# Kernel tuning notes

Hardware: AMD Instinct MI355X
Metric: run time of the kernel (lower is better)

The kernel has to match this reference:

```python
import jax, jax.numpy as jnp
import numpy as np

NUM_RBF = 16
TOP_K = 32
MAX_REL = 32  # max_relative_feature


def _rbf(D):
    # D: [...,] -> [..., NUM_RBF]
    mu = jnp.linspace(2.0, 22.0, NUM_RBF)
    sigma = (22.0 - 2.0) / NUM_RBF
    return jnp.exp(-(((D[..., None] - mu) / sigma) ** 2))


def _gather_nodes(x, idx):
    # x: [B, N, ...], idx: [B, N, K] -> [B, N, K, ...]
    return jax.vmap(lambda xb, ib: xb[ib])(x, idx)


def _forward(X, mask, residue_idx, chain_labels, W_pos, b_pos, W_edge, ln_gamma, ln_beta):
    N_at = X[:, :, 0, :]
    C = X[:, :, 1, :]
    Ca = X[:, :, 2, :]
    O = X[:, :, 3, :]
    b = Ca - N_at
    c = C - Ca
    a = jnp.cross(b, c)
    Cb = -0.58273431 * a + 0.56802827 * b - 0.54067466 * c + Ca

    # --- _dist: masked pairwise distances on C atoms + topk neighbor search ---
    mask2 = mask[:, :, None] * mask[:, None, :]              # [B,N,N]
    dX = C[:, None, :, :] - C[:, :, None, :]                 # [B,N,N,3]
    D = mask2 * jnp.sqrt(jnp.sum(dX ** 2, -1) + 1e-6)
    D_max = jnp.max(D, -1, keepdims=True)
    D_adjust = D + (1.0 - mask2) * D_max
    neg_vals, E_idx = jax.lax.top_k(-D_adjust, TOP_K)        # smallest distances
    D_neighbors = -neg_vals                                  # [B,N,K]

    # --- 25 RBF distance features (1 from topk + 24 atom-pair gathers) ---
    atoms = {'N': N_at, 'C': C, 'Ca': Ca, 'Cb': Cb, 'O': O}
    pairs = [('N','N'),('Ca','Ca'),('Cb','Cb'),('C','N'),('C','Ca'),('C','Cb'),
             ('N','Ca'),('N','Cb'),('Cb','Ca'),('N','C'),('Ca','C'),('Cb','C'),
             ('Ca','N'),('Cb','N'),('Ca','Cb'),('O','O'),('C','O'),('O','C'),
             ('N','O'),('O','N'),('Cb','O'),('O','Ca'),('O','Cb'),('Ca','O')]
    A_all = jnp.stack([atoms[p[0]] for p in pairs])          # [P,B,N,3]
    B_all = jnp.stack([atoms[p[1]] for p in pairs])          # [P,B,N,3]
    B_nb = jax.vmap(_gather_nodes, in_axes=(0, None))(B_all, E_idx)  # [P,B,N,K,3]
    D_pair = jnp.sqrt(jnp.sum((A_all[:, :, :, None, :] - B_nb) ** 2, -1) + 1e-6)  # [P,B,N,K]
    RBF_pairs = _rbf(D_pair)                                 # [P,B,N,K,R]
    Bsz, Nres, K = E_idx.shape
    RBF_all = jnp.concatenate(
        [_rbf(D_neighbors), jnp.moveaxis(RBF_pairs, 0, 3).reshape(Bsz, Nres, K, -1)], -1)

    # --- positional encodings (relative residue index, chain mask) ---
    r_nb = _gather_nodes(residue_idx, E_idx)                 # [B,N,K]
    offset = residue_idx[:, :, None] - r_nb
    c_nb = _gather_nodes(chain_labels, E_idx)
    E_chains = (chain_labels[:, :, None] == c_nb).astype(jnp.int32)
    d = jnp.clip(offset + MAX_REL, 0, 2 * MAX_REL) * E_chains + (1 - E_chains) * (2 * MAX_REL + 1)
    E_pos = W_pos[d] + b_pos                                 # one_hot @ W == table lookup

    # --- edge embedding + LayerNorm ---
    E = jnp.concatenate([E_pos, RBF_all], -1)                # [B,N,K,416]
    E = E @ W_edge                                           # [B,N,K,128]
    mu = jnp.mean(E, -1, keepdims=True)
    var = jnp.var(E, -1, keepdims=True)
    E = (E - mu) / jnp.sqrt(var + 1e-5) * ln_gamma + ln_beta
    return E, E_idx


def setup_inputs() -> dict:
    key = jax.random.key(0)
    ks = jax.random.split(key, 6)
    B, N = 4, 2048
    edge_in = 16 + NUM_RBF * 25  # 416
    X = jax.random.normal(ks[0], (B, N, 4, 3), dtype=jnp.float32) * 10.0
    mask = jnp.ones((B, N), dtype=jnp.float32)
    residue_idx = jnp.broadcast_to(jnp.arange(N, dtype=jnp.int32), (B, N))
    chain_labels = jax.random.randint(ks[1], (B, N), 0, 2).astype(jnp.int32)
    W_pos = jax.random.normal(ks[2], (2 * MAX_REL + 2, 16), dtype=jnp.float32) * 0.05
    b_pos = jnp.zeros((16,), dtype=jnp.float32)
    W_edge = jax.random.normal(ks[3], (edge_in, 128), dtype=jnp.float32) * 0.05
    ln_gamma = jnp.ones((128,), dtype=jnp.float32)
    ln_beta = jnp.zeros((128,), dtype=jnp.float32)
    return {"X": X, "mask": mask, "residue_idx": residue_idx, "chain_labels": chain_labels,
            "W_pos": W_pos, "b_pos": b_pos, "W_edge": W_edge,
            "ln_gamma": ln_gamma, "ln_beta": ln_beta}


def reference(X, mask, residue_idx, chain_labels, W_pos, b_pos, W_edge, ln_gamma, ln_beta):
    return _forward(X, mask, residue_idx, chain_labels, W_pos, b_pos, W_edge, ln_gamma, ln_beta)
```

## Files before the change

### kernel.cpp

```cpp
#include <hip/hip_runtime.h>
#include <math.h>

#define BB 4
#define NN 2048
#define KK 32
#define COUT 128
#define KT 13
#define NBIN 512
#define SCAP 512
#define TGN 4096
#define CHA 7
#define CHB 6

typedef __attribute__((ext_vector_type(8))) short bf16x8;
typedef __attribute__((ext_vector_type(4))) float f32x4;
typedef unsigned long long ull;

constexpr int PA_E[12] = {0,3,1,0,3,2,2,2,1,0,3,4};
constexpr int PB_E[12] = {0,3,2,2,2,1,0,3,4,4,4,3};
constexpr int PA_O[12] = {2,1,1,0,0,3,3,4,4,4,4,2};
constexpr int PB_O[12] = {2,0,3,3,1,1,0,4,1,0,2,4};

__device__ inline ushort f2bf(float x) {
    unsigned u = __float_as_uint(x);
    unsigned r = (u + 0x7FFFu + ((u >> 16) & 1u)) >> 16;
    return (ushort)r;
}

__global__ __launch_bounds__(256) void prep_kernel(
    const float* __restrict__ X, const float* __restrict__ W,
    const float* __restrict__ Wpos, const float* __restrict__ bpos,
    ushort* __restrict__ Wsw, uint4* __restrict__ rbfTab,
    ushort* __restrict__ WposBf, float4* __restrict__ Ccomp) {
    int blk = blockIdx.x, tid = threadIdx.x;
    if (blk < 26) {
        int t = blk * 256 + tid;
        int lane = t & 63;
        int ct = (t >> 6) & 7;
        int kt = t >> 9;
        int k0 = kt * 32 + (lane >> 4) * 8;
        int col = ct * 16 + (lane & 15);
        ushort o[8];
#pragma unroll
        for (int i = 0; i < 8; i++) o[i] = f2bf(W[(k0 + i) * COUT + col]);
        *reinterpret_cast<uint4*>(Wsw + (size_t)t * 8) = *reinterpret_cast<uint4*>(o);
    } else if (blk < 42) {
        int g = (blk - 26) * 256 + tid;
        float d = ((float)g + 0.5f) * (1.0f / 128.0f);
        unsigned w[8];
#pragma unroll
        for (int i2 = 0; i2 < 8; i2++) {
            float mu0 = 2.0f + (20.0f / 15.0f) * (float)(2 * i2);
            float mu1 = 2.0f + (20.0f / 15.0f) * (float)(2 * i2 + 1);
            float u0 = (d - mu0) * 0.8f;
            float u1 = (d - mu1) * 0.8f;
            float e0 = __expf(-u0 * u0);
            float e1 = __expf(-u1 * u1);
            w[i2] = ((__float_as_uint(e0) + 0x8000u) >> 16) |
                    ((__float_as_uint(e1) + 0x8000u) & 0xFFFF0000u);
        }
        rbfTab[g * 2 + 0] = make_uint4(w[0], w[1], w[2], w[3]);
        rbfTab[g * 2 + 1] = make_uint4(w[4], w[5], w[6], w[7]);
    } else if (blk < 47) {
        int t = (blk - 42) * 256 + tid;
        if (t < 66 * 16) {
            int c = t & 15;
            WposBf[t] = f2bf(Wpos[t] + bpos[c]);
        }
    } else {
        int i = (blk - 47) * 256 + tid;
        const float4* p4 = (const float4*)(X + (size_t)i * 12);
        float4 f0 = p4[0], f1 = p4[1];
        Ccomp[i] = make_float4(f0.w, f1.x, f1.y, 0.0f);
    }
}

__global__ __launch_bounds__(256) void topk_kernel(const float4* __restrict__ Ccomp,
                                                   int* __restrict__ eidx,
                                                   float* __restrict__ dnb,
                                                   float* __restrict__ out_idx) {
    __shared__ unsigned hist[NBIN];
    __shared__ ull surv[SCAP];
    __shared__ unsigned wcnt[4][8];
    int bid = blockIdx.x;
    int b = bid >> 11;
    int n = bid & (NN - 1);
    int tid = threadIdx.x;
    const int wv = tid >> 6, lane = tid & 63;

    hist[tid] = 0;
    hist[tid + 256] = 0;
    __syncthreads();

    const float4* cb = Ccomp + (size_t)b * NN;
    float4 s = cb[n];
    ull key[8];
    int bin[8];
#pragma unroll
    for (int i = 0; i < 8; i++) {
        int j = i * 256 + tid;
        float4 c = cb[j];
        float dx = c.x - s.x, dy = c.y - s.y, dz = c.z - s.z;
        float d = sqrtf(dx * dx + dy * dy + dz * dz + 1e-6f);
        key[i] = ((ull)__float_as_uint(d) << 32) | (unsigned)j;
        bin[i] = (int)fminf(d * 8.0f, (float)(NBIN - 1));
        atomicAdd(&hist[bin[i]], 1u);
    }
    __syncthreads();

    if (tid < 64) {
        int base = tid * 8;
        unsigned h[8];
        unsigned tot = 0;
#pragma unroll
        for (int i = 0; i < 8; i++) { h[i] = hist[base + i]; tot += h[i]; }
        unsigned sc = tot;
#pragma unroll
        for (int off = 1; off <= 32; off <<= 1) {
            unsigned o = __shfl_up(sc, off);
            if (tid >= off) sc += o;
        }
        unsigned run = sc - tot;
#pragma unroll
        for (int i = 0; i < 8; i++) {
            unsigned c = h[i];
            hist[base + i] = run;
            run += c;
        }
    }
    __syncthreads();

    ull blt[8];
#pragma unroll
    for (int i = 0; i < 8; i++) {
        blt[i] = __ballot(hist[bin[i]] < KK);
    }
    if (lane == 0) {
#pragma unroll
        for (int i = 0; i < 8; i++) wcnt[wv][i] = (unsigned)__popcll(blt[i]);
    }
    __syncthreads();

    unsigned mybase[8];
    unsigned run = 0;
#pragma unroll
    for (int i = 0; i < 8; i++) {
#pragma unroll
        for (int w = 0; w < 4; w++) {
            if (w == wv) mybase[i] = run;
            run += wcnt[w][i];
        }
    }
    const ull ltm = (1ULL << lane) - 1ULL;
#pragma unroll
    for (int i = 0; i < 8; i++) {
        if (hist[bin[i]] < KK) {
            unsigned pos = mybase[i] + (unsigned)__popcll(blt[i] & ltm);
            if (pos < SCAP) surv[pos] = key[i];
        }
    }
    int sv = (int)(run < SCAP ? run : SCAP);
    __syncthreads();

    for (int i = tid; i < sv; i += 256) {
        ull k = surv[i];
        int rank = 0;
        for (int t = 0; t < sv; ++t) rank += (surv[t] < k) ? 1 : 0;
        if (rank < KK) {
            int j = (int)(unsigned)(k & 0xffffffffu);
            float d = __uint_as_float((unsigned)(k >> 32));
            size_t o = (size_t)bid * KK + rank;
            eidx[o] = j;
            dnb[o] = d;
            out_idx[o] = (float)j;
        }
    }
}

__global__ __launch_bounds__(512, 4) void edge_kernel(
    const float* __restrict__ X, const int* __restrict__ eidx,
    const float* __restrict__ dnb, const int* __restrict__ ridx,
    const int* __restrict__ clab, const ushort* __restrict__ WposBf,
    const ushort* __restrict__ Wsw, const uint4* __restrict__ rbfTab,
    const float* __restrict__ gamma, const float* __restrict__ beta,
    float* __restrict__ Eout, float* __restrict__ outIdx) {
    __shared__ ushort wbuf[CHA * 4096];

    const int tid = threadIdx.x;
    const int wv = tid >> 6, lane = tid & 63;
    const int node = blockIdx.x * 8 + wv;
    const int bbase = node & ~(NN - 1);
    const int q = lane >> 4, r = lane & 15;
    const int h = q & 1, par = q >> 1;

    auto stage = [&](int k0, int nk) {
        for (int p = 0; p < nk; p++) {
            const ushort* src = Wsw + (k0 + p) * 4096 + tid * 8;
            ushort* dst = &wbuf[p * 4096 + wv * 512];
            __builtin_amdgcn_global_load_lds(
                (const __attribute__((address_space(1))) unsigned int*)src,
                (__attribute__((address_space(3))) unsigned int*)dst, 16, 0, 0);
        }
    };
    stage(0, CHA);

    const int erow0 = node * KK + r;
    const int erow1 = node * KK + 16 + r;
    const int j0 = eidx[(size_t)erow0];
    const int j1 = eidx[(size_t)erow1];

    auto loadAtoms = [&](int i, float* A) {
        const float4* p4 = (const float4*)(X + (size_t)i * 12);
        float4 f0 = p4[0], f1 = p4[1], f2 = p4[2];
        A[0] = f0.x;  A[1] = f0.y;  A[2] = f0.z;
        A[3] = f0.w;  A[4] = f1.x;  A[5] = f1.y;
        A[6] = f1.z;  A[7] = f1.w;  A[8] = f2.x;
        A[12] = f2.y; A[13] = f2.z; A[14] = f2.w;
        float bx = A[6] - A[0], by = A[7] - A[1], bz = A[8] - A[2];
        float cx = A[3] - A[6], cy = A[4] - A[7], cz = A[5] - A[8];
        float ax = by * cz - bz * cy;
        float ay = bz * cx - bx * cz;
        float az = bx * cy - by * cx;
        A[9]  = -0.58273431f * ax + 0.56802827f * bx - 0.54067466f * cx + A[6];
        A[10] = -0.58273431f * ay + 0.56802827f * by - 0.54067466f * cy + A[7];
        A[11] = -0.58273431f * az + 0.56802827f * bz - 0.54067466f * cz + A[8];
        A[15] = 0.0f;
    };
    float S[16], R0[16], R1[16];
    loadAtoms(node, S);
    loadAtoms(bbase + j0, R0);
    loadAtoms(bbase + j1, R1);

    float d0[12], d1[12];
#define DIST12(PAx, PBx)                                                          \
    {                                                                             \
        _Pragma("unroll") for (int t = 0; t < 12; t++) {                          \
            const int ia = PAx[t] * 3, ib = PBx[t] * 3;                           \
            float dx = S[ia] - R0[ib], dy = S[ia + 1] - R0[ib + 1],               \
                  dz = S[ia + 2] - R0[ib + 2];                                    \
            d0[t] = sqrtf(dx * dx + dy * dy + dz * dz + 1e-6f);                   \
            dx = S[ia] - R1[ib]; dy = S[ia + 1] - R1[ib + 1];                     \
            dz = S[ia + 2] - R1[ib + 2];                                          \
            d1[t] = sqrtf(dx * dx + dy * dy + dz * dz + 1e-6f);                   \
        }                                                                         \
    }
    if (par == 0) DIST12(PA_E, PB_E) else DIST12(PA_O, PB_O)
#undef DIST12

    union U8 { uint4 u4; bf16x8 v; };
    auto rbf8 = [&](float d) -> bf16x8 {
        int idx = (int)fminf(d * 128.0f, (float)(TGN - 1));
        U8 o;
        o.u4 = rbfTab[idx * 2 + h];
        return o.v;
    };
    bf16x8 a00, a10;
    if (q < 2) {
        int off0 = ridx[node] - ridx[bbase + j0];
        int dd0 = off0 + 32; dd0 = dd0 < 0 ? 0 : (dd0 > 64 ? 64 : dd0);
        int dpos0 = (clab[node] == clab[bbase + j0]) ? dd0 : 65;
        int off1 = ridx[node] - ridx[bbase + j1];
        int dd1 = off1 + 32; dd1 = dd1 < 0 ? 0 : (dd1 > 64 ? 64 : dd1);
        int dpos1 = (clab[node] == clab[bbase + j1]) ? dd1 : 65;
        U8 aE0, aE1;
        aE0.u4 = *(const uint4*)(WposBf + dpos0 * 16 + 8 * h);
        aE1.u4 = *(const uint4*)(WposBf + dpos1 * 16 + 8 * h);
        a00 = aE0.v; a10 = aE1.v;
    } else {
        a00 = rbf8(dnb[(size_t)erow0]);
        a10 = rbf8(dnb[(size_t)erow1]);
    }

    f32x4 acc0[8], acc1[8];
#pragma unroll
    for (int ct = 0; ct < 8; ct++) {
        acc0[ct] = (f32x4){0.f, 0.f, 0.f, 0.f};
        acc1[ct] = (f32x4){0.f, 0.f, 0.f, 0.f};
    }
    const ushort* bs = wbuf + lane * 8;
    __syncthreads();
#pragma unroll
    for (int kt = 0; kt < CHA; kt++) {
        bf16x8 a0, a1;
        if (kt == 0) { a0 = a00; a1 = a10; }
        else         { a0 = rbf8(d0[kt - 1]); a1 = rbf8(d1[kt - 1]); }
#pragma unroll
        for (int ct = 0; ct < 8; ct++) {
            bf16x8 w = *(const bf16x8*)(bs + kt * 4096 + ct * 512);
            acc0[ct] = __builtin_amdgcn_mfma_f32_16x16x32_bf16(w, a0, acc0[ct], 0, 0, 0);
            acc1[ct] = __builtin_amdgcn_mfma_f32_16x16x32_bf16(w, a1, acc1[ct], 0, 0, 0);
        }
    }
    __syncthreads();
    stage(CHA, CHB);
    __syncthreads();
#pragma unroll
    for (int kt = CHA; kt < KT; kt++) {
        bf16x8 a0 = rbf8(d0[kt - 1]);
        bf16x8 a1 = rbf8(d1[kt - 1]);
#pragma unroll
        for (int ct = 0; ct < 8; ct++) {
            bf16x8 w = *(const bf16x8*)(bs + (kt - CHA) * 4096 + ct * 512);
            acc0[ct] = __builtin_amdgcn_mfma_f32_16x16x32_bf16(w, a0, acc0[ct], 0, 0, 0);
            acc1[ct] = __builtin_amdgcn_mfma_f32_16x16x32_bf16(w, a1, acc1[ct], 0, 0, 0);
        }
    }

    float s1a = 0.f, s2a = 0.f, s1b = 0.f, s2b = 0.f;
#pragma unroll
    for (int ct = 0; ct < 8; ct++) {
#pragma unroll
        for (int i = 0; i < 4; i++) {
            float v0 = acc0[ct][i];
            float v1 = acc1[ct][i];
            s1a += v0; s2a += v0 * v0;
            s1b += v1; s2b += v1 * v1;
        }
    }
    s1a += __shfl_xor(s1a, 16); s2a += __shfl_xor(s2a, 16);
    s1a += __shfl_xor(s1a, 32); s2a += __shfl_xor(s2a, 32);
    s1b += __shfl_xor(s1b, 16); s2b += __shfl_xor(s2b, 16);
    s1b += __shfl_xor(s1b, 32); s2b += __shfl_xor(s2b, 32);
    float meanA = s1a * (1.0f / 128.0f);
    float varA = s2a * (1.0f / 128.0f) - meanA * meanA;
    float rstdA = rsqrtf(varA + 1e-5f);
    float meanB = s1b * (1.0f / 128.0f);
    float varB = s2b * (1.0f / 128.0f) - meanB * meanB;
    float rstdB = rsqrtf(varB + 1e-5f);

    float* orow0 = Eout + (size_t)erow0 * COUT + q * 4;
    float* orow1 = Eout + (size_t)erow1 * COUT + q * 4;
#pragma unroll
    for (int ct = 0; ct < 8; ct++) {
        float4 g4 = *(const float4*)(gamma + ct * 16 + q * 4);
        float4 b4 = *(const float4*)(beta + ct * 16 + q * 4);
        float4 oa, ob;
        oa.x = (acc0[ct][0] - meanA) * rstdA * g4.x + b4.x;
        oa.y = (acc0[ct][1] - meanA) * rstdA * g4.y + b4.y;
        oa.z = (acc0[ct][2] - meanA) * rstdA * g4.z + b4.z;
        oa.w = (acc0[ct][3] - meanA) * rstdA * g4.w + b4.w;
        ob.x = (acc1[ct][0] - meanB) * rstdB * g4.x + b4.x;
        ob.y = (acc1[ct][1] - meanB) * rstdB * g4.y + b4.y;
        ob.z = (acc1[ct][2] - meanB) * rstdB * g4.z + b4.z;
        ob.w = (acc1[ct][3] - meanB) * rstdB * g4.w + b4.w;
        *(float4*)(orow0 + ct * 16) = oa;
        *(float4*)(orow1 + ct * 16) = ob;
    }

    if (q == 0) {
        outIdx[(size_t)erow0] = (float)j0;
        outIdx[(size_t)erow1] = (float)j1;
    }
}

extern "C" void kernel_launch(void* const* d_in, const int* in_sizes, int n_in,
                              void* d_out, int out_size, void* d_ws, size_t ws_size,
                              hipStream_t stream) {
    const float* X = (const float*)d_in[0];
    const int* ridx = (const int*)d_in[2];
    const int* clab = (const int*)d_in[3];
    const float* Wpos = (const float*)d_in[4];
    const float* bpos = (const float*)d_in[5];
    const float* Wedge = (const float*)d_in[6];
    const float* gamma = (const float*)d_in[7];
    const float* beta = (const float*)d_in[8];

    float* out = (float*)d_out;
    float* E = out;
    float* outidx = out + (size_t)BB * NN * KK * COUT;

    char* ws = (char*)d_ws;
    uint4* rbfTab = (uint4*)ws;
    ushort* Wsw = (ushort*)(ws + 131072);
    ushort* WposBf = (ushort*)(ws + 131072 + 106496);
    float4* Ccomp = (float4*)(ws + 131072 + 106496 + 2112);
    int* eidx = (int*)(ws + 131072 + 106496 + 2112 + 131072);
    float* dnbuf = (float*)(ws + 131072 + 106496 + 2112 + 131072 + 1048576);

    prep_kernel<<<79, 256, 0, stream>>>(X, Wedge, Wpos, bpos, Wsw, rbfTab,
                                        WposBf, Ccomp);
    topk_kernel<<<BB * NN, 256, 0, stream>>>(Ccomp, eidx, dnbuf, outidx);
    edge_kernel<<<BB * NN / 8, 512, 0, stream>>>(X, eidx, dnbuf, ridx, clab,
                                                 WposBf, Wsw, rbfTab, gamma, beta,
                                                 E, outidx);
}
```

Baseline: 90.84 us.

## Overlap weight prep with topk and double-buffer edge kernel weight staging

The weight swizzle, RBF table and positional-table prep move out of the first kernel and into extra blocks at the end of the topk grid, leaving a tiny Ccomp-only kernel on the critical path. In the edge kernel, the second weight chunk goes into a separate LDS buffer and is staged before the first chunk's MFMAs, so its load overlaps compute instead of following a barrier. All RBF table lookups are also hoisted into registers ahead of the MFMA loop. The cost is more LDS and registers per block, with launch bounds lowered from 4 to 2 blocks per CU, which cuts occupancy.

Measured after the change: 103.7 us. +14.2%, slower.

```diff
diff --git a/kernel.cpp b/kernel.cpp
--- a/kernel.cpp
+++ b/kernel.cpp
@@ -9,8 +9,7 @@
 #define NBIN 512
 #define SCAP 512
 #define TGN 4096
-#define CHA 7
-#define CHB 6
+#define NTOPK (BB * NN)
 
 typedef __attribute__((ext_vector_type(8))) short bf16x8;
 typedef __attribute__((ext_vector_type(4))) float f32x4;
@@ -27,65 +26,68 @@
     return (ushort)r;
 }
 
-__global__ __launch_bounds__(256) void prep_kernel(
-    const float* __restrict__ X, const float* __restrict__ W,
+__global__ __launch_bounds__(256) void ccomp_kernel(const float* __restrict__ X,
+                                                    float4* __restrict__ Ccomp) {
+    int i = blockIdx.x * 256 + threadIdx.x;
+    const float4* p4 = (const float4*)(X + (size_t)i * 12);
+    float4 f0 = p4[0], f1 = p4[1];
+    Ccomp[i] = make_float4(f0.w, f1.x, f1.y, 0.0f);
+}
+
+__global__ __launch_bounds__(256) void topk_kernel(
+    const float4* __restrict__ Ccomp, const float* __restrict__ W,
     const float* __restrict__ Wpos, const float* __restrict__ bpos,
     ushort* __restrict__ Wsw, uint4* __restrict__ rbfTab,
-    ushort* __restrict__ WposBf, float4* __restrict__ Ccomp) {
-    int blk = blockIdx.x, tid = threadIdx.x;
-    if (blk < 26) {
-        int t = blk * 256 + tid;
-        int lane = t & 63;
-        int ct = (t >> 6) & 7;
-        int kt = t >> 9;
-        int k0 = kt * 32 + (lane >> 4) * 8;
-        int col = ct * 16 + (lane & 15);
-        ushort o[8];
-#pragma unroll
-        for (int i = 0; i < 8; i++) o[i] = f2bf(W[(k0 + i) * COUT + col]);
-        *reinterpret_cast<uint4*>(Wsw + (size_t)t * 8) = *reinterpret_cast<uint4*>(o);
-    } else if (blk < 42) {
-        int g = (blk - 26) * 256 + tid;
-        float d = ((float)g + 0.5f) * (1.0f / 128.0f);
-        unsigned w[8];
-#pragma unroll
-        for (int i2 = 0; i2 < 8; i2++) {
-            float mu0 = 2.0f + (20.0f / 15.0f) * (float)(2 * i2);
-            float mu1 = 2.0f + (20.0f / 15.0f) * (float)(2 * i2 + 1);
-            float u0 = (d - mu0) * 0.8f;
-            float u1 = (d - mu1) * 0.8f;
-            float e0 = __expf(-u0 * u0);
-            float e1 = __expf(-u1 * u1);
-            w[i2] = ((__float_as_uint(e0) + 0x8000u) >> 16) |
-                    ((__float_as_uint(e1) + 0x8000u) & 0xFFFF0000u);
-        }
-        rbfTab[g * 2 + 0] = make_uint4(w[0], w[1], w[2], w[3]);
-        rbfTab[g * 2 + 1] = make_uint4(w[4], w[5], w[6], w[7]);
-    } else if (blk < 47) {
-        int t = (blk - 42) * 256 + tid;
-        if (t < 66 * 16) {
-            int c = t & 15;
-            WposBf[t] = f2bf(Wpos[t] + bpos[c]);
-        }
-    } else {
-        int i = (blk - 47) * 256 + tid;
-        const float4* p4 = (const float4*)(X + (size_t)i * 12);
-        float4 f0 = p4[0], f1 = p4[1];
-        Ccomp[i] = make_float4(f0.w, f1.x, f1.y, 0.0f);
-    }
-}
-
-__global__ __launch_bounds__(256) void topk_kernel(const float4* __restrict__ Ccomp,
-                                                   int* __restrict__ eidx,
-                                                   float* __restrict__ dnb,
-                                                   float* __restrict__ out_idx) {
+    ushort* __restrict__ WposBf, int* __restrict__ eidx,
+    float* __restrict__ dnb, float* __restrict__ out_idx) {
+    int bid = blockIdx.x;
+    int tid = threadIdx.x;
+
+    if (bid >= NTOPK) {
+        int blk = bid - NTOPK;
+        if (blk < 26) {
+            int t = blk * 256 + tid;
+            int lane = t & 63;
+            int ct = (t >> 6) & 7;
+            int kt = t >> 9;
+            int k0 = kt * 32 + (lane >> 4) * 8;
+            int col = ct * 16 + (lane & 15);
+            ushort o[8];
+#pragma unroll
+            for (int i = 0; i < 8; i++) o[i] = f2bf(W[(k0 + i) * COUT + col]);
+            *reinterpret_cast<uint4*>(Wsw + (size_t)t * 8) = *reinterpret_cast<uint4*>(o);
+        } else if (blk < 42) {
+            int g = (blk - 26) * 256 + tid;
+            float d = ((float)g + 0.5f) * (1.0f / 128.0f);
+            unsigned w[8];
+#pragma unroll
+            for (int i2 = 0; i2 < 8; i2++) {
+                float mu0 = 2.0f + (20.0f / 15.0f) * (float)(2 * i2);
+                float mu1 = 2.0f + (20.0f / 15.0f) * (float)(2 * i2 + 1);
+                float u0 = (d - mu0) * 0.8f;
+                float u1 = (d - mu1) * 0.8f;
+                float e0 = __expf(-u0 * u0);
+                float e1 = __expf(-u1 * u1);
+                w[i2] = ((__float_as_uint(e0) + 0x8000u) >> 16) |
+                        ((__float_as_uint(e1) + 0x8000u) & 0xFFFF0000u);
+            }
+            rbfTab[g * 2 + 0] = make_uint4(w[0], w[1], w[2], w[3]);
+            rbfTab[g * 2 + 1] = make_uint4(w[4], w[5], w[6], w[7]);
+        } else {
+            int t = (blk - 42) * 256 + tid;
+            if (t < 66 * 16) {
+                int c = t & 15;
+                WposBf[t] = f2bf(Wpos[t] + bpos[c]);
+            }
+        }
+        return;
+    }
+
     __shared__ unsigned hist[NBIN];
     __shared__ ull surv[SCAP];
     __shared__ unsigned wcnt[4][8];
-    int bid = blockIdx.x;
     int b = bid >> 11;
     int n = bid & (NN - 1);
-    int tid = threadIdx.x;
     const int wv = tid >> 6, lane = tid & 63;
 
     hist[tid] = 0;
@@ -177,14 +179,15 @@
     }
 }
 
-__global__ __launch_bounds__(512, 4) void edge_kernel(
+__global__ __launch_bounds__(512, 2) void edge_kernel(
     const float* __restrict__ X, const int* __restrict__ eidx,
     const float* __restrict__ dnb, const int* __restrict__ ridx,
     const int* __restrict__ clab, const ushort* __restrict__ WposBf,
     const ushort* __restrict__ Wsw, const uint4* __restrict__ rbfTab,
     const float* __restrict__ gamma, const float* __restrict__ beta,
     float* __restrict__ Eout, float* __restrict__ outIdx) {
-    __shared__ ushort wbuf[CHA * 4096];
+    __shared__ ushort bufA[7 * 4096];
+    __shared__ ushort bufB[6 * 4096];
 
     const int tid = threadIdx.x;
     const int wv = tid >> 6, lane = tid & 63;
@@ -193,16 +196,16 @@
     const int q = lane >> 4, r = lane & 15;
     const int h = q & 1, par = q >> 1;
 
-    auto stage = [&](int k0, int nk) {
+    auto stage = [&](int k0, int nk, ushort* buf) {
         for (int p = 0; p < nk; p++) {
             const ushort* src = Wsw + (k0 + p) * 4096 + tid * 8;
-            ushort* dst = &wbuf[p * 4096 + wv * 512];
+            ushort* dst = &buf[p * 4096 + wv * 512];
             __builtin_amdgcn_global_load_lds(
                 (const __attribute__((address_space(1))) unsigned int*)src,
                 (__attribute__((address_space(3))) unsigned int*)dst, 16, 0, 0);
         }
     };
-    stage(0, CHA);
+    stage(0, 7, bufA);
 
     const int erow0 = node * KK + r;
     const int erow1 = node * KK + 16 + r;
@@ -248,13 +251,7 @@
 #undef DIST12
 
     union U8 { uint4 u4; bf16x8 v; };
-    auto rbf8 = [&](float d) -> bf16x8 {
-        int idx = (int)fminf(d * 128.0f, (float)(TGN - 1));
-        U8 o;
-        o.u4 = rbfTab[idx * 2 + h];
-        return o.v;
-    };
-    bf16x8 a00, a10;
+    uint4 fr0[KT], fr1[KT];
     if (q < 2) {
         int off0 = ridx[node] - ridx[bbase + j0];
         int dd0 = off0 + 32; dd0 = dd0 < 0 ? 0 : (dd0 > 64 ? 64 : dd0);
@@ -262,13 +259,20 @@
         int off1 = ridx[node] - ridx[bbase + j1];
         int dd1 = off1 + 32; dd1 = dd1 < 0 ? 0 : (dd1 > 64 ? 64 : dd1);
         int dpos1 = (clab[node] == clab[bbase + j1]) ? dd1 : 65;
-        U8 aE0, aE1;
-        aE0.u4 = *(const uint4*)(WposBf + dpos0 * 16 + 8 * h);
-        aE1.u4 = *(const uint4*)(WposBf + dpos1 * 16 + 8 * h);
-        a00 = aE0.v; a10 = aE1.v;
+        fr0[0] = *(const uint4*)(WposBf + dpos0 * 16 + 8 * h);
+        fr1[0] = *(const uint4*)(WposBf + dpos1 * 16 + 8 * h);
     } else {
-        a00 = rbf8(dnb[(size_t)erow0]);
-        a10 = rbf8(dnb[(size_t)erow1]);
+        int i0 = (int)fminf(dnb[(size_t)erow0] * 128.0f, (float)(TGN - 1));
+        int i1 = (int)fminf(dnb[(size_t)erow1] * 128.0f, (float)(TGN - 1));
+        fr0[0] = rbfTab[i0 * 2 + h];
+        fr1[0] = rbfTab[i1 * 2 + h];
+    }
+#pragma unroll
+    for (int kt = 1; kt < KT; kt++) {
+        int i0 = (int)fminf(d0[kt - 1] * 128.0f, (float)(TGN - 1));
+        int i1 = (int)fminf(d1[kt - 1] * 128.0f, (float)(TGN - 1));
+        fr0[kt] = rbfTab[i0 * 2 + h];
+        fr1[kt] = rbfTab[i1 * 2 + h];
     }
 
     f32x4 acc0[8], acc1[8];
@@ -277,32 +281,33 @@
         acc0[ct] = (f32x4){0.f, 0.f, 0.f, 0.f};
         acc1[ct] = (f32x4){0.f, 0.f, 0.f, 0.f};
     }
-    const ushort* bs = wbuf + lane * 8;
-    __syncthreads();
-#pragma unroll
-    for (int kt = 0; kt < CHA; kt++) {
-        bf16x8 a0, a1;
-        if (kt == 0) { a0 = a00; a1 = a10; }
-        else         { a0 = rbf8(d0[kt - 1]); a1 = rbf8(d1[kt - 1]); }
-#pragma unroll
-        for (int ct = 0; ct < 8; ct++) {
-            bf16x8 w = *(const bf16x8*)(bs + kt * 4096 + ct * 512);
-            acc0[ct] = __builtin_amdgcn_mfma_f32_16x16x32_bf16(w, a0, acc0[ct], 0, 0, 0);
-            acc1[ct] = __builtin_amdgcn_mfma_f32_16x16x32_bf16(w, a1, acc1[ct], 0, 0, 0);
-        }
-    }
-    __syncthreads();
-    stage(CHA, CHB);
-    __syncthreads();
-#pragma unroll
-    for (int kt = CHA; kt < KT; kt++) {
-        bf16x8 a0 = rbf8(d0[kt - 1]);
-        bf16x8 a1 = rbf8(d1[kt - 1]);
-#pragma unroll
-        for (int ct = 0; ct < 8; ct++) {
-            bf16x8 w = *(const bf16x8*)(bs + (kt - CHA) * 4096 + ct * 512);
-            acc0[ct] = __builtin_amdgcn_mfma_f32_16x16x32_bf16(w, a0, acc0[ct], 0, 0, 0);
-            acc1[ct] = __builtin_amdgcn_mfma_f32_16x16x32_bf16(w, a1, acc1[ct], 0, 0, 0);
+    __syncthreads();
+    stage(7, 6, bufB);
+    {
+        const ushort* bs = bufA + lane * 8;
+#pragma unroll
+        for (int kt = 0; kt < 7; kt++) {
+            U8 a0u, a1u; a0u.u4 = fr0[kt]; a1u.u4 = fr1[kt];
+#pragma unroll
+            for (int ct = 0; ct < 8; ct++) {
+                bf16x8 w = *(const bf16x8*)(bs + kt * 4096 + ct * 512);
+                acc0[ct] = __builtin_amdgcn_mfma_f32_16x16x32_bf16(w, a0u.v, acc0[ct], 0, 0, 0);
+                acc1[ct] = __builtin_amdgcn_mfma_f32_16x16x32_bf16(w, a1u.v, acc1[ct], 0, 0, 0);
+            }
+        }
+    }
+    __syncthreads();
+    {
+        const ushort* bs = bufB + lane * 8;
+#pragma unroll
+        for (int kt = 7; kt < KT; kt++) {
+            U8 a0u, a1u; a0u.u4 = fr0[kt]; a1u.u4 = fr1[kt];
+#pragma unroll
+            for (int ct = 0; ct < 8; ct++) {
+                bf16x8 w = *(const bf16x8*)(bs + (kt - 7) * 4096 + ct * 512);
+                acc0[ct] = __builtin_amdgcn_mfma_f32_16x16x32_bf16(w, a0u.v, acc0[ct], 0, 0, 0);
+                acc1[ct] = __builtin_amdgcn_mfma_f32_16x16x32_bf16(w, a1u.v, acc1[ct], 0, 0, 0);
+            }
         }
     }
 
@@ -377,9 +382,9 @@
     int* eidx = (int*)(ws + 131072 + 106496 + 2112 + 131072);
     float* dnbuf = (float*)(ws + 131072 + 106496 + 2112 + 131072 + 1048576);
 
-    prep_kernel<<<79, 256, 0, stream>>>(X, Wedge, Wpos, bpos, Wsw, rbfTab,
-                                        WposBf, Ccomp);
-    topk_kernel<<<BB * NN, 256, 0, stream>>>(Ccomp, eidx, dnbuf, outidx);
+    ccomp_kernel<<<32, 256, 0, stream>>>(X, Ccomp);
+    topk_kernel<<<NTOPK + 47, 256, 0, stream>>>(Ccomp, Wedge, Wpos, bpos, Wsw,
+                                                rbfTab, WposBf, eidx, dnbuf, outidx);
     edge_kernel<<<BB * NN / 8, 512, 0, stream>>>(X, eidx, dnbuf, ridx, clab,
                                                  WposBf, Wsw, rbfTab, gamma, beta,
                                                  E, outidx);
```
